# Optimization experiments

Measured on AMD Instinct MI355X. Metric: run time of the kernel, lower is better.

The kernel has to match this reference:

```python
import jax, jax.numpy as jnp
import numpy as np
import math

D_EMBED = 128   # per-head dim (config.d_embed)
N_HEADS = 12
ROPE_BASE = 10000.0


def rope(x):
    # x: [B, H, S, D]; interleaved-pair rotary embedding on last dim
    B, H, S, D = x.shape
    half = D // 2
    inv_freq = 1.0 / (ROPE_BASE ** (jnp.arange(0, half, dtype=jnp.float32) * 2.0 / D))
    ang = jnp.arange(S, dtype=jnp.float32)[:, None] * inv_freq[None, :]  # [S, D/2]
    cos, sin = jnp.cos(ang), jnp.sin(ang)
    xp = x.reshape(B, H, S, half, 2)
    x1, x2 = xp[..., 0], xp[..., 1]
    o1 = x1 * cos - x2 * sin
    o2 = x1 * sin + x2 * cos
    return jnp.stack([o1, o2], axis=-1).reshape(B, H, S, D)


def setup_inputs() -> dict:
    key = jax.random.key(0)
    ks = jax.random.split(key, 5)
    B, S, E = 2, 2048, D_EMBED // 2
    inner = N_HEADS * D_EMBED
    sc = 0.02
    return {
        "q": jax.random.normal(ks[0], (B, S, E), dtype=jnp.float32),
        "Wq": jax.random.normal(ks[1], (inner, E), dtype=jnp.float32) * sc,
        "Wk": jax.random.normal(ks[2], (inner, E), dtype=jnp.float32) * sc,
        "Wv": jax.random.normal(ks[3], (inner, E), dtype=jnp.float32) * sc,
        "Wo": jax.random.normal(ks[4], (E, inner), dtype=jnp.float32) * sc,
    }


def reference(q, Wq, Wk, Wv, Wo):
    B, S, E = q.shape
    H, D = N_HEADS, D_EMBED
    scale = 1.0 / math.sqrt(D)

    def proj(x, W):
        return (x @ W.T).reshape(B, S, H, D).transpose(0, 2, 1, 3)  # [B,H,S,D]

    qh = rope(proj(q, Wq))
    kh = rope(proj(q, Wk))
    vh = proj(q, Wv)

    scores = jnp.einsum("bhsd,bhtd->bhst", qh, kh) * scale  # [B,H,S,S]
    causal = jnp.tril(jnp.ones((S, S), dtype=bool))
    scores = jnp.where(causal, scores, -jnp.inf)
    probs = jax.nn.softmax(scores, axis=-1)  # dropout omitted (eval mode)
    out = jnp.einsum("bhst,bhtd->bhsd", probs, vh)
    out = out.transpose(0, 2, 1, 3).reshape(B, S, H * D)
    return out @ Wo.T  # [B,S,E]
```

## Files before the change

kernel.cpp:

```cpp
#include <hip/hip_runtime.h>
#include <stdint.h>


typedef short v8s __attribute__((ext_vector_type(8)));
typedef unsigned int v4u __attribute__((ext_vector_type(4)));
typedef float v4f __attribute__((ext_vector_type(4)));
typedef float v16f __attribute__((ext_vector_type(16)));

#define MFMA16(a, b, c) __builtin_amdgcn_mfma_f32_16x16x32_bf16(a, b, c, 0, 0, 0)
#define MFMA32(a, b, c) __builtin_amdgcn_mfma_f32_32x32x16_bf16(a, b, c, 0, 0, 0)

#if __has_builtin(__builtin_amdgcn_exp2f)
#define EXP2(x) __builtin_amdgcn_exp2f(x)
#else
#define EXP2(x) exp2f(x)
#endif

#define SCALE2 (0.08838834764831845f * 1.4426950408889634f)

__device__ __forceinline__ unsigned short f2bf(float f) {
  uint32_t u = __builtin_bit_cast(uint32_t, f);
  u += 0x7FFFu + ((u >> 16) & 1u);
  return (unsigned short)(u >> 16);
}

__device__ __forceinline__ uint32_t packbf(float lo, float hi) {
  return __builtin_amdgcn_perm(__builtin_bit_cast(uint32_t, hi) + 0x8000u,
                               __builtin_bit_cast(uint32_t, lo) + 0x8000u,
                               0x07060302u);
}

__device__ __forceinline__ v16f zero16() {
  v16f z;
#pragma unroll
  for (int i = 0; i < 16; ++i) z[i] = 0.f;
  return z;
}

__device__ __forceinline__ void gl_lds16(const unsigned short* g, unsigned short* l) {
  __builtin_amdgcn_global_load_lds(
      (const __attribute__((address_space(1))) uint32_t*)g,
      (__attribute__((address_space(3))) uint32_t*)l, 16, 0, 0);
}

__global__ __launch_bounds__(256) void rope_table(float* __restrict__ cos_t,
                                                  float* __restrict__ sin_t) {
  int idx = blockIdx.x * 256 + threadIdx.x;
  if (idx >= 2048 * 64) return;
  int s = idx >> 6, f = idx & 63;
  float inv = exp2f((float)f * -0.20762050593046014f);
  float ang = (float)s * inv;
  float si, co;
  sincosf(ang, &si, &co);
  cos_t[idx] = co;
  sin_t[idx] = si;
}

__global__ __launch_bounds__(256) void proj_rope(
    const float* __restrict__ x, const float* __restrict__ Wq,
    const float* __restrict__ Wk, const float* __restrict__ Wv,
    const float* __restrict__ cos_t, const float* __restrict__ sin_t,
    unsigned short* __restrict__ qh, unsigned short* __restrict__ kh,
    unsigned short* __restrict__ vt) {
  const int wave = threadIdx.x >> 6, lane = threadIdx.x & 63;
  const int l16 = lane & 15, quad = lane >> 4;
  const int by = blockIdx.y;
  const int o_base = by * 64 + wave * 16;
  const int mat = o_base / 1536;
  const int inner0 = o_base % 1536;
  const int d0w = inner0 & 127;
  const float* Wsrc = (mat == 0) ? Wq : ((mat == 1) ? Wk : Wv);
  const float qscale = (mat == 0) ? SCALE2 : 1.0f;

  __shared__ __align__(16) unsigned short Lt[64][72];

  v8s wb[2];
  {
    const float* wr = Wsrc + (size_t)(inner0 + l16) * 64 + quad * 8;
#pragma unroll
    for (int s = 0; s < 2; ++s) {
      float4 a = *(const float4*)(wr + s * 32);
      float4 b = *(const float4*)(wr + s * 32 + 4);
      v8s t;
      t[0] = (short)f2bf(a.x); t[1] = (short)f2bf(a.y);
      t[2] = (short)f2bf(a.z); t[3] = (short)f2bf(a.w);
      t[4] = (short)f2bf(b.x); t[5] = (short)f2bf(b.y);
      t[6] = (short)f2bf(b.z); t[7] = (short)f2bf(b.w);
      wb[s] = t;
    }
  }

  const int d = d0w + l16;
  const int half = d >> 1;

#pragma unroll
  for (int i = 0; i < 4; ++i) {
    const int tok0 = blockIdx.x * 64 + i * 16;
    const float* xr = x + (size_t)(tok0 + l16) * 64 + quad * 8;
    v8s xa[2];
#pragma unroll
    for (int s = 0; s < 2; ++s) {
      float4 a = *(const float4*)(xr + s * 32);
      float4 b = *(const float4*)(xr + s * 32 + 4);
      v8s t;
      t[0] = (short)f2bf(a.x); t[1] = (short)f2bf(a.y);
      t[2] = (short)f2bf(a.z); t[3] = (short)f2bf(a.w);
      t[4] = (short)f2bf(b.x); t[5] = (short)f2bf(b.y);
      t[6] = (short)f2bf(b.z); t[7] = (short)f2bf(b.w);
      xa[s] = t;
    }
    v4f acc = {0.f, 0.f, 0.f, 0.f};
    acc = MFMA16(xa[0], wb[0], acc);
    acc = MFMA16(xa[1], wb[1], acc);

    if (mat < 2) {
#pragma unroll
      for (int r = 0; r < 4; ++r) {
        int sidx = (tok0 + quad * 4 + r) & 2047;
        float val = acc[r];
        float prt = __shfl_xor(val, 1);
        float co = cos_t[sidx * 64 + half];
        float si = sin_t[sidx * 64 + half];
        float rot = ((d & 1) == 0) ? (val * co - prt * si)
                                   : (prt * si + val * co);
        Lt[i * 16 + quad * 4 + r][wave * 16 + l16] = f2bf(rot * qscale);
      }
    } else {
#pragma unroll
      for (int r = 0; r < 4; ++r)
        Lt[wave * 16 + l16][i * 16 + quad * 4 + r] = f2bf(acc[r]);
    }
  }
  __syncthreads();

  const int matb = (by * 64) / 1536;
  const int innerb = (by * 64) % 1536;
  const int hb = innerb >> 7;
  const int d0b = innerb & 127;
  const int b = (blockIdx.x * 64) >> 11;
  const int tokbase = (blockIdx.x * 64) & 2047;
#pragma unroll
  for (int jj = 0; jj < 2; ++jj) {
    int cid = jj * 256 + threadIdx.x;
    int outer = cid >> 3, ic = cid & 7;
    v8s val = *(const v8s*)&Lt[outer][ic * 8];
    if (matb < 2) {
      unsigned short* dst = (matb == 0 ? qh : kh) +
          (((size_t)(b * 12 + hb)) * 2048 + tokbase + outer) * 128 + d0b + ic * 8;
      *(v8s*)dst = val;
    } else {
      unsigned short* dst = vt +
          (((size_t)(b * 12 + hb)) * 128 + d0b + outer) * 2048 + tokbase + ic * 8;
      *(v8s*)dst = val;
    }
  }
}

__global__ __launch_bounds__(256, 2) void attn(
    const unsigned short* __restrict__ qh, const unsigned short* __restrict__ kh,
    const unsigned short* __restrict__ vt, unsigned short* __restrict__ att,
    const float* __restrict__ Wo, unsigned short* __restrict__ wob) {
  const int bh = blockIdx.x;
  const int qb = 15 - (int)blockIdx.y;
  const int t = threadIdx.x;
  const int lane = t & 63;
  const int l31 = lane & 31, hh = lane >> 5;
  const int w = t >> 6;
  const int r0w = qb * 128 + w * 32;
  const int qrow = r0w + l31;
  const int rowmax = r0w + 31;

  const unsigned short* Qb = qh + (size_t)bh * 2048 * 128;
  const unsigned short* Kb = kh + (size_t)bh * 2048 * 128;
  const unsigned short* Vb = vt + (size_t)bh * 128 * 2048;

  __shared__ __align__(16) unsigned short Ktile[2][64 * 128];
  __shared__ __align__(16) unsigned short Vtile[2][128 * 64];

  v8s qa[8];
  {
    const unsigned short* qr = Qb + (size_t)(r0w + l31) * 128 + hh * 8;
#pragma unroll
    for (int ks = 0; ks < 8; ++ks) qa[ks] = *(const v8s*)(qr + ks * 16);
  }

  int offK[4], offV[4], ldsO[4];
#pragma unroll
  for (int j = 0; j < 4; ++j) {
    int flat = j * 256 + t;
    int kr = flat >> 4, kc = flat & 15;
    offK[j] = kr * 128 + ((kc ^ (kr & 15)) << 3);
    int vd = flat >> 3, vc = flat & 7;
    offV[j] = vd * 2048 + ((vc ^ (vd & 7)) << 3);
    ldsO[j] = flat << 3;
  }
  auto stage = [&](int kt, int buf) {
    const int key0 = kt << 6;
    const unsigned short* kg = Kb + (size_t)key0 * 128;
    const unsigned short* vg = Vb + key0;
#pragma unroll
    for (int j = 0; j < 4; ++j) {
      gl_lds16(kg + offK[j], &Ktile[buf][ldsO[j]]);
      gl_lds16(vg + offV[j], &Vtile[buf][ldsO[j]]);
    }
  };

  v16f O[4];
#pragma unroll
  for (int i = 0; i < 4; ++i) O[i] = zero16();
  float lsum = 0.f;

  const int nkt = 2 * qb + 2;
  stage(0, 0);

  for (int kt = 0; kt < nkt; ++kt) {
    __syncthreads();
    if (kt + 1 < nkt) stage(kt + 1, (kt + 1) & 1);
    const int key0 = kt << 6;
    if (key0 > rowmax) continue;
    const unsigned short* Kl = Ktile[kt & 1];
    const unsigned short* Vl = Vtile[kt & 1];
    const bool hi = (key0 + 32) <= rowmax;
    const bool mask0 = (key0 + 31) > r0w;
    const bool mask1 = (key0 + 63) > r0w;

    auto softpack = [&](const v16f& S, int kh2, bool needmask, uint32_t* W) {
#pragma unroll
      for (int m = 0; m < 8; ++m) {
        float pa = EXP2(S[2 * m]);
        float pb = EXP2(S[2 * m + 1]);
        if (needmask) {
          int keyb = key0 + kh2 * 32 + 2 * (m & 1) + 8 * (m >> 1) + 4 * hh;
          pa = (keyb <= qrow) ? pa : 0.f;
          pb = (keyb + 1 <= qrow) ? pb : 0.f;
        }
        lsum += pa + pb;
        W[m] = packbf(pa, pb);
      }
    };
    auto pv = [&](const uint32_t* W, int kh2) {
      uint32_t r0 = __shfl_xor(hh ? W[0] : W[2], 32);
      uint32_t r1 = __shfl_xor(hh ? W[1] : W[3], 32);
      uint32_t r2 = __shfl_xor(hh ? W[4] : W[6], 32);
      uint32_t r3 = __shfl_xor(hh ? W[5] : W[7], 32);
#pragma unroll
      for (int gl = 0; gl < 2; ++gl) {
        const int g = kh2 * 2 + gl;
        if (key0 + g * 16 > rowmax) continue;
        uint32_t rA = gl ? r2 : r0, rB = gl ? r3 : r1;
        v4u fw;
        fw.x = hh ? rA : W[4 * gl];
        fw.y = hh ? rB : W[4 * gl + 1];
        fw.z = hh ? W[4 * gl + 2] : rA;
        fw.w = hh ? W[4 * gl + 3] : rB;
        v8s pb = __builtin_bit_cast(v8s, fw);
#pragma unroll
        for (int dt = 0; dt < 4; ++dt) {
          v8s va = *(const v8s*)(
              Vl + (((dt * 32 + l31) * 8 + ((2 * g + hh) ^ (l31 & 7))) << 3));
          O[dt] = MFMA32(va, pb, O[dt]);
        }
      }
    };

    v16f S0 = zero16();
#pragma unroll
    for (int ks = 0; ks < 8; ++ks) {
      v8s ka = *(const v8s*)(
          Kl + ((l31 * 16 + ((2 * ks + hh) ^ (l31 & 15))) << 3));
      S0 = MFMA32(ka, qa[ks], S0);
    }
    uint32_t W0[8];
    softpack(S0, 0, mask0, W0);
    pv(W0, 0);
    if (hi) {
      v16f S1 = zero16();
#pragma unroll
      for (int ks = 0; ks < 8; ++ks) {
        v8s ka = *(const v8s*)(
            Kl + (((32 + l31) * 16 + ((2 * ks + hh) ^ (l31 & 15))) << 3));
        S1 = MFMA32(ka, qa[ks], S1);
      }
      uint32_t W1[8];
      softpack(S1, 1, mask1, W1);
      pv(W1, 1);
    }
  }

  float tot = lsum + __shfl_xor(lsum, 32);
  float inv = 1.0f / tot;
  const int b = bh / 12, hq = bh % 12;
  unsigned short* arow = att + ((size_t)b * 2048 + qrow) * 1536 + hq * 128;
#pragma unroll
  for (int dt = 0; dt < 4; ++dt) {
#pragma unroll
    for (int pr = 0; pr < 4; ++pr) {
      float a0 = O[dt][4 * pr + 0] * inv, a1 = O[dt][4 * pr + 1] * inv;
      float a2 = O[dt][4 * pr + 2] * inv, a3 = O[dt][4 * pr + 3] * inv;
      uint2 uu;
      uu.x = packbf(a0, a1);
      uu.y = packbf(a2, a3);
      *(uint2*)(arow + dt * 32 + 8 * pr + 4 * hh) = uu;
    }
  }

  if (qb == 0) {
    const int base = bh * 4096;
#pragma unroll
    for (int i = 0; i < 16; ++i) wob[base + i * 256 + t] = f2bf(Wo[base + i * 256 + t]);
  }
}

__global__ __launch_bounds__(256) void outproj(
    const unsigned short* __restrict__ att, const unsigned short* __restrict__ wob,
    float* __restrict__ out) {
  const int wave = threadIdx.x >> 6, lane = threadIdx.x & 63;
  const int l16 = lane & 15, quad = lane >> 4;
  const int tok0 = blockIdx.x * 16;
  const int e0 = wave * 16;

  v4f acc0 = {0.f, 0.f, 0.f, 0.f}, acc1 = {0.f, 0.f, 0.f, 0.f};
  const unsigned short* ar = att + (size_t)(tok0 + l16) * 1536 + quad * 8;
  const unsigned short* wr = wob + (size_t)(e0 + l16) * 1536 + quad * 8;
#pragma unroll 4
  for (int s = 0; s < 24; ++s) {
    v8s a0 = *(const v8s*)(ar + (2 * s) * 32);
    v8s b0 = *(const v8s*)(wr + (2 * s) * 32);
    v8s a1 = *(const v8s*)(ar + (2 * s + 1) * 32);
    v8s b1 = *(const v8s*)(wr + (2 * s + 1) * 32);
    acc0 = MFMA16(a0, b0, acc0);
    acc1 = MFMA16(a1, b1, acc1);
  }
#pragma unroll
  for (int r = 0; r < 4; ++r)
    out[(size_t)(tok0 + quad * 4 + r) * 64 + e0 + l16] = acc0[r] + acc1[r];
}

extern "C" void kernel_launch(void* const* d_in, const int* in_sizes, int n_in,
                              void* d_out, int out_size, void* d_ws,
                              size_t ws_size, hipStream_t stream) {
  const float* q  = (const float*)d_in[0];
  const float* Wq = (const float*)d_in[1];
  const float* Wk = (const float*)d_in[2];
  const float* Wv = (const float*)d_in[3];
  const float* Wo = (const float*)d_in[4];
  float* out = (float*)d_out;

  unsigned short* ws = (unsigned short*)d_ws;
  unsigned short* qh  = ws;
  unsigned short* kh  = ws + 6291456;
  unsigned short* vt  = ws + 12582912;
  unsigned short* att = ws + 18874368;
  float* cos_t = (float*)((char*)d_ws + 50331648);
  float* sin_t = cos_t + 131072;
  unsigned short* wob = (unsigned short*)cos_t;

  rope_table<<<512, 256, 0, stream>>>(cos_t, sin_t);
  proj_rope<<<dim3(64, 72), 256, 0, stream>>>(q, Wq, Wk, Wv, cos_t, sin_t,
                                              qh, kh, vt);
  attn<<<dim3(24, 16), 256, 0, stream>>>(qh, kh, vt, att, Wo, wob);
  outproj<<<256, 256, 0, stream>>>(att, wob, out);
}
```

Before: 194.4 us.

## Split attention into 64-row query blocks with 32-key tiles and balanced scheduling

Shrinks attention work-groups from 4 to 2 waves covering 64 query rows, so the grid grows from 384 to 768 blocks. A remapped block index orders query blocks so heavy and light causal blocks are interleaved across the launch. Key/value tiles are halved to 32 keys with adjusted LDS swizzles. The QK^T accumulation is split into two independent MFMA chains to expose more ILP. This aims at better CU occupancy and load balance on the causal triangle, at the cost of more K/V reloads per query row and more barriers.

```diff
diff --git a/kernel.cpp b/kernel.cpp
--- a/kernel.cpp
+++ b/kernel.cpp
@@ -156,17 +156,19 @@
   }
 }
 
-__global__ __launch_bounds__(256, 2) void attn(
+__global__ __launch_bounds__(128, 2) void attn(
     const unsigned short* __restrict__ qh, const unsigned short* __restrict__ kh,
     const unsigned short* __restrict__ vt, unsigned short* __restrict__ att,
     const float* __restrict__ Wo, unsigned short* __restrict__ wob) {
-  const int bh = blockIdx.x;
-  const int qb = 15 - (int)blockIdx.y;
+  const int n = blockIdx.x;
+  const int bh = n % 24;
+  const int y = n / 24;
+  const int j = (y >= 11 && y < 22) ? (y - 1) : (31 - y);
   const int t = threadIdx.x;
   const int lane = t & 63;
   const int l31 = lane & 31, hh = lane >> 5;
   const int w = t >> 6;
-  const int r0w = qb * 128 + w * 32;
+  const int r0w = j * 64 + w * 32;
   const int qrow = r0w + l31;
   const int rowmax = r0w + 31;
 
@@ -174,8 +176,8 @@
   const unsigned short* Kb = kh + (size_t)bh * 2048 * 128;
   const unsigned short* Vb = vt + (size_t)bh * 128 * 2048;
 
-  __shared__ __align__(16) unsigned short Ktile[2][64 * 128];
-  __shared__ __align__(16) unsigned short Vtile[2][128 * 64];
+  __shared__ __align__(16) unsigned short Ktile[2][32 * 128];
+  __shared__ __align__(16) unsigned short Vtile[2][128 * 32];
 
   v8s qa[8];
   {
@@ -186,22 +188,22 @@
 
   int offK[4], offV[4], ldsO[4];
 #pragma unroll
-  for (int j = 0; j < 4; ++j) {
-    int flat = j * 256 + t;
+  for (int i = 0; i < 4; ++i) {
+    int flat = i * 128 + t;
     int kr = flat >> 4, kc = flat & 15;
-    offK[j] = kr * 128 + ((kc ^ (kr & 15)) << 3);
-    int vd = flat >> 3, vc = flat & 7;
-    offV[j] = vd * 2048 + ((vc ^ (vd & 7)) << 3);
-    ldsO[j] = flat << 3;
+    offK[i] = kr * 128 + ((kc ^ (kr & 15)) << 3);
+    int vd = flat >> 2, vc = flat & 3;
+    offV[i] = vd * 2048 + ((vc ^ ((vd >> 1) & 3)) << 3);
+    ldsO[i] = flat << 3;
   }
   auto stage = [&](int kt, int buf) {
-    const int key0 = kt << 6;
+    const int key0 = kt << 5;
     const unsigned short* kg = Kb + (size_t)key0 * 128;
     const unsigned short* vg = Vb + key0;
 #pragma unroll
-    for (int j = 0; j < 4; ++j) {
-      gl_lds16(kg + offK[j], &Ktile[buf][ldsO[j]]);
-      gl_lds16(vg + offV[j], &Vtile[buf][ldsO[j]]);
+    for (int i = 0; i < 4; ++i) {
+      gl_lds16(kg + offK[i], &Ktile[buf][ldsO[i]]);
+      gl_lds16(vg + offV[i], &Vtile[buf][ldsO[i]]);
     }
   };
 
@@ -210,80 +212,63 @@
   for (int i = 0; i < 4; ++i) O[i] = zero16();
   float lsum = 0.f;
 
-  const int nkt = 2 * qb + 2;
+  const int nkt = 2 * j + 2;
   stage(0, 0);
 
   for (int kt = 0; kt < nkt; ++kt) {
     __syncthreads();
     if (kt + 1 < nkt) stage(kt + 1, (kt + 1) & 1);
-    const int key0 = kt << 6;
+    const int key0 = kt << 5;
     if (key0 > rowmax) continue;
     const unsigned short* Kl = Ktile[kt & 1];
     const unsigned short* Vl = Vtile[kt & 1];
-    const bool hi = (key0 + 32) <= rowmax;
     const bool mask0 = (key0 + 31) > r0w;
-    const bool mask1 = (key0 + 63) > r0w;
-
-    auto softpack = [&](const v16f& S, int kh2, bool needmask, uint32_t* W) {
-#pragma unroll
-      for (int m = 0; m < 8; ++m) {
-        float pa = EXP2(S[2 * m]);
-        float pb = EXP2(S[2 * m + 1]);
-        if (needmask) {
-          int keyb = key0 + kh2 * 32 + 2 * (m & 1) + 8 * (m >> 1) + 4 * hh;
-          pa = (keyb <= qrow) ? pa : 0.f;
-          pb = (keyb + 1 <= qrow) ? pb : 0.f;
-        }
-        lsum += pa + pb;
-        W[m] = packbf(pa, pb);
+
+    v16f Sa = zero16(), Sb = zero16();
+#pragma unroll
+    for (int ks = 0; ks < 8; ks += 2) {
+      v8s ka0 = *(const v8s*)(
+          Kl + ((l31 * 16 + ((2 * ks + hh) ^ (l31 & 15))) << 3));
+      v8s ka1 = *(const v8s*)(
+          Kl + ((l31 * 16 + ((2 * ks + 2 + hh) ^ (l31 & 15))) << 3));
+      Sa = MFMA32(ka0, qa[ks], Sa);
+      Sb = MFMA32(ka1, qa[ks + 1], Sb);
+    }
+
+    uint32_t W[8];
+#pragma unroll
+    for (int m = 0; m < 8; ++m) {
+      float pa = EXP2(Sa[2 * m] + Sb[2 * m]);
+      float pb = EXP2(Sa[2 * m + 1] + Sb[2 * m + 1]);
+      if (mask0) {
+        int keyb = key0 + 2 * (m & 1) + 8 * (m >> 1) + 4 * hh;
+        pa = (keyb <= qrow) ? pa : 0.f;
+        pb = (keyb + 1 <= qrow) ? pb : 0.f;
       }
-    };
-    auto pv = [&](const uint32_t* W, int kh2) {
-      uint32_t r0 = __shfl_xor(hh ? W[0] : W[2], 32);
-      uint32_t r1 = __shfl_xor(hh ? W[1] : W[3], 32);
-      uint32_t r2 = __shfl_xor(hh ? W[4] : W[6], 32);
-      uint32_t r3 = __shfl_xor(hh ? W[5] : W[7], 32);
-#pragma unroll
-      for (int gl = 0; gl < 2; ++gl) {
-        const int g = kh2 * 2 + gl;
-        if (key0 + g * 16 > rowmax) continue;
-        uint32_t rA = gl ? r2 : r0, rB = gl ? r3 : r1;
-        v4u fw;
-        fw.x = hh ? rA : W[4 * gl];
-        fw.y = hh ? rB : W[4 * gl + 1];
-        fw.z = hh ? W[4 * gl + 2] : rA;
-        fw.w = hh ? W[4 * gl + 3] : rB;
-        v8s pb = __builtin_bit_cast(v8s, fw);
-#pragma unroll
-        for (int dt = 0; dt < 4; ++dt) {
-          v8s va = *(const v8s*)(
-              Vl + (((dt * 32 + l31) * 8 + ((2 * g + hh) ^ (l31 & 7))) << 3));
-          O[dt] = MFMA32(va, pb, O[dt]);
-        }
+      lsum += pa + pb;
+      W[m] = packbf(pa, pb);
+    }
+
+    uint32_t r0 = __shfl_xor(hh ? W[0] : W[2], 32);
+    uint32_t r1 = __shfl_xor(hh ? W[1] : W[3], 32);
+    uint32_t r2 = __shfl_xor(hh ? W[4] : W[6], 32);
+    uint32_t r3 = __shfl_xor(hh ? W[5] : W[7], 32);
+#pragma unroll
+    for (int g = 0; g < 2; ++g) {
+      if (key0 + g * 16 > rowmax) continue;
+      uint32_t rA = g ? r2 : r0, rB = g ? r3 : r1;
+      v4u fw;
+      fw.x = hh ? rA : W[4 * g];
+      fw.y = hh ? rB : W[4 * g + 1];
+      fw.z = hh ? W[4 * g + 2] : rA;
+      fw.w = hh ? W[4 * g + 3] : rB;
+      v8s pfrag = __builtin_bit_cast(v8s, fw);
+#pragma unroll
+      for (int dt = 0; dt < 4; ++dt) {
+        v8s va = *(const v8s*)(
+            Vl + (((dt * 32 + l31) * 4 + ((2 * g + hh) ^ ((l31 >> 1) & 3))) << 3));
+        O[dt] = MFMA32(va, pfrag, O[dt]);
       }
-    };
-
-    v16f S0 = zero16();
-#pragma unroll
-    for (int ks = 0; ks < 8; ++ks) {
-      v8s ka = *(const v8s*)(
-          Kl + ((l31 * 16 + ((2 * ks + hh) ^ (l31 & 15))) << 3));
-      S0 = MFMA32(ka, qa[ks], S0);
-    }
-    uint32_t W0[8];
-    softpack(S0, 0, mask0, W0);
-    pv(W0, 0);
-    if (hi) {
-      v16f S1 = zero16();
-#pragma unroll
-      for (int ks = 0; ks < 8; ++ks) {
-        v8s ka = *(const v8s*)(
-            Kl + (((32 + l31) * 16 + ((2 * ks + hh) ^ (l31 & 15))) << 3));
-        S1 = MFMA32(ka, qa[ks], S1);
-      }
-      uint32_t W1[8];
-      softpack(S1, 1, mask1, W1);
-      pv(W1, 1);
     }
   }
 
@@ -304,10 +289,10 @@
     }
   }
 
-  if (qb == 0) {
+  if (j == 0) {
     const int base = bh * 4096;
 #pragma unroll
-    for (int i = 0; i < 16; ++i) wob[base + i * 256 + t] = f2bf(Wo[base + i * 256 + t]);
+    for (int i = 0; i < 32; ++i) wob[base + i * 128 + t] = f2bf(Wo[base + i * 128 + t]);
   }
 }
 
@@ -358,6 +343,6 @@
   rope_table<<<512, 256, 0, stream>>>(cos_t, sin_t);
   proj_rope<<<dim3(64, 72), 256, 0, stream>>>(q, Wq, Wk, Wv, cos_t, sin_t,
                                               qh, kh, vt);
-  attn<<<dim3(24, 16), 256, 0, stream>>>(qh, kh, vt, att, Wo, wob);
+  attn<<<dim3(768), 128, 0, stream>>>(qh, kh, vt, att, Wo, wob);
   outproj<<<256, 256, 0, stream>>>(att, wob, out);
 }
```

Result: slower. 208.6 us (+7.3%).

## Prepack V into MFMA fragment layout and load directly to registers; triple-buffer K

Applied to the files above, without the earlier changes.

The projection kernel now writes V in a fragment-major layout so each attention wave can fetch its PV operands straight from global memory into registers, skipping the LDS V tile entirely. K staging becomes a three-deep ring with explicit vmcnt waits and a raw s_barrier instead of __syncthreads, which lets loads run two tiles ahead. The QK^T chain is split into two independent accumulators to shorten the MFMA dependency chain, and s_setprio is raised around the MFMA blocks. The risks are redundant global V reads across the four waves, more register pressure from the prefetched V fragments, and fragile hand-written wait counts.

```diff
diff --git a/kernel.cpp b/kernel.cpp
--- a/kernel.cpp
+++ b/kernel.cpp
@@ -149,8 +149,12 @@
           (((size_t)(b * 12 + hb)) * 2048 + tokbase + outer) * 128 + d0b + ic * 8;
       *(v8s*)dst = val;
     } else {
+      const int kt = tokbase >> 6;
+      const int G = ic >> 1, hhb = ic & 1;
+      const int dd = d0b + outer;
       unsigned short* dst = vt +
-          (((size_t)(b * 12 + hb)) * 128 + d0b + outer) * 2048 + tokbase + ic * 8;
+          ((((((size_t)(b * 12 + hb)) * 32 + kt) * 4 + G) * 4 + (dd >> 5)) * 64 +
+           hhb * 32 + (dd & 31)) * 8;
       *(v8s*)dst = val;
     }
   }
@@ -158,7 +162,7 @@
 
 __global__ __launch_bounds__(256, 2) void attn(
     const unsigned short* __restrict__ qh, const unsigned short* __restrict__ kh,
-    const unsigned short* __restrict__ vt, unsigned short* __restrict__ att,
+    const unsigned short* __restrict__ vtf, unsigned short* __restrict__ att,
     const float* __restrict__ Wo, unsigned short* __restrict__ wob) {
   const int bh = blockIdx.x;
   const int qb = 15 - (int)blockIdx.y;
@@ -172,10 +176,9 @@
 
   const unsigned short* Qb = qh + (size_t)bh * 2048 * 128;
   const unsigned short* Kb = kh + (size_t)bh * 2048 * 128;
-  const unsigned short* Vb = vt + (size_t)bh * 128 * 2048;
-
-  __shared__ __align__(16) unsigned short Ktile[2][64 * 128];
-  __shared__ __align__(16) unsigned short Vtile[2][128 * 64];
+  const unsigned short* Vb = vtf + (size_t)bh * 262144;
+
+  __shared__ __align__(16) unsigned short Ktile[3][64 * 128];
 
   v8s qa[8];
   {
@@ -184,25 +187,18 @@
     for (int ks = 0; ks < 8; ++ks) qa[ks] = *(const v8s*)(qr + ks * 16);
   }
 
-  int offK[4], offV[4], ldsO[4];
-#pragma unroll
-  for (int j = 0; j < 4; ++j) {
-    int flat = j * 256 + t;
+  int offK[4], ldsO[4];
+#pragma unroll
+  for (int i = 0; i < 4; ++i) {
+    int flat = i * 256 + t;
     int kr = flat >> 4, kc = flat & 15;
-    offK[j] = kr * 128 + ((kc ^ (kr & 15)) << 3);
-    int vd = flat >> 3, vc = flat & 7;
-    offV[j] = vd * 2048 + ((vc ^ (vd & 7)) << 3);
-    ldsO[j] = flat << 3;
-  }
-  auto stage = [&](int kt, int buf) {
-    const int key0 = kt << 6;
-    const unsigned short* kg = Kb + (size_t)key0 * 128;
-    const unsigned short* vg = Vb + key0;
-#pragma unroll
-    for (int j = 0; j < 4; ++j) {
-      gl_lds16(kg + offK[j], &Ktile[buf][ldsO[j]]);
-      gl_lds16(vg + offV[j], &Vtile[buf][ldsO[j]]);
-    }
+    offK[i] = kr * 128 + ((kc ^ (kr & 15)) << 3);
+    ldsO[i] = flat << 3;
+  }
+  auto stageK = [&](int kt, int buf) {
+    const unsigned short* kg = Kb + ((size_t)(kt << 6)) * 128;
+#pragma unroll
+    for (int i = 0; i < 4; ++i) gl_lds16(kg + offK[i], &Ktile[buf][ldsO[i]]);
   };
 
   v16f O[4];
@@ -211,24 +207,56 @@
   float lsum = 0.f;
 
   const int nkt = 2 * qb + 2;
-  stage(0, 0);
+  stageK(0, 0);
+  stageK(1, 1);
+  asm volatile("s_waitcnt vmcnt(4)" ::: "memory");
 
   for (int kt = 0; kt < nkt; ++kt) {
-    __syncthreads();
-    if (kt + 1 < nkt) stage(kt + 1, (kt + 1) & 1);
+    __builtin_amdgcn_s_barrier();
+    __builtin_amdgcn_sched_barrier(0);
     const int key0 = kt << 6;
-    if (key0 > rowmax) continue;
-    const unsigned short* Kl = Ktile[kt & 1];
-    const unsigned short* Vl = Vtile[kt & 1];
+    const bool active = key0 <= rowmax;
     const bool hi = (key0 + 32) <= rowmax;
+
+    v8s v0a[4], v0b[4], v1a[4], v1b[4];
+    if (active) {
+      const unsigned short* Vt = Vb + (size_t)kt * 8192;
+#pragma unroll
+      for (int dt = 0; dt < 4; ++dt)
+        v0a[dt] = *(const v8s*)(Vt + ((0 * 4 + dt) * 64 + lane) * 8);
+#pragma unroll
+      for (int dt = 0; dt < 4; ++dt)
+        v0b[dt] = *(const v8s*)(Vt + ((1 * 4 + dt) * 64 + lane) * 8);
+      if (hi) {
+#pragma unroll
+        for (int dt = 0; dt < 4; ++dt)
+          v1a[dt] = *(const v8s*)(Vt + ((2 * 4 + dt) * 64 + lane) * 8);
+#pragma unroll
+        for (int dt = 0; dt < 4; ++dt)
+          v1b[dt] = *(const v8s*)(Vt + ((3 * 4 + dt) * 64 + lane) * 8);
+      }
+    }
+    __builtin_amdgcn_sched_barrier(0);
+
+    if (kt + 2 < nkt) stageK(kt + 2, (kt + 2) % 3);
+    __builtin_amdgcn_sched_barrier(0);
+
+    if (!active) {
+      if (kt + 2 < nkt) asm volatile("s_waitcnt vmcnt(4)" ::: "memory");
+      else              asm volatile("s_waitcnt vmcnt(0)" ::: "memory");
+      continue;
+    }
+
+    const unsigned short* Kl = Ktile[kt % 3];
     const bool mask0 = (key0 + 31) > r0w;
     const bool mask1 = (key0 + 63) > r0w;
 
-    auto softpack = [&](const v16f& S, int kh2, bool needmask, uint32_t* W) {
+    auto softpack = [&](const v16f& SS, const v16f& ST, int kh2, bool needmask,
+                        uint32_t* W) {
 #pragma unroll
       for (int m = 0; m < 8; ++m) {
-        float pa = EXP2(S[2 * m]);
-        float pb = EXP2(S[2 * m + 1]);
+        float pa = EXP2(SS[2 * m] + ST[2 * m]);
+        float pb = EXP2(SS[2 * m + 1] + ST[2 * m + 1]);
         if (needmask) {
           int keyb = key0 + kh2 * 32 + 2 * (m & 1) + 8 * (m >> 1) + 4 * hh;
           pa = (keyb <= qrow) ? pa : 0.f;
@@ -238,7 +266,7 @@
         W[m] = packbf(pa, pb);
       }
     };
-    auto pv = [&](const uint32_t* W, int kh2) {
+    auto pvhalf = [&](const uint32_t* W, int kh2, const v8s* vA, const v8s* vB) {
       uint32_t r0 = __shfl_xor(hh ? W[0] : W[2], 32);
       uint32_t r1 = __shfl_xor(hh ? W[1] : W[3], 32);
       uint32_t r2 = __shfl_xor(hh ? W[4] : W[6], 32);
@@ -253,37 +281,47 @@
         fw.y = hh ? rB : W[4 * gl + 1];
         fw.z = hh ? W[4 * gl + 2] : rA;
         fw.w = hh ? W[4 * gl + 3] : rB;
-        v8s pb = __builtin_bit_cast(v8s, fw);
-#pragma unroll
-        for (int dt = 0; dt < 4; ++dt) {
-          v8s va = *(const v8s*)(
-              Vl + (((dt * 32 + l31) * 8 + ((2 * g + hh) ^ (l31 & 7))) << 3));
-          O[dt] = MFMA32(va, pb, O[dt]);
-        }
+        v8s pfrag = __builtin_bit_cast(v8s, fw);
+        const v8s* vv = gl ? vB : vA;
+        __builtin_amdgcn_s_setprio(1);
+#pragma unroll
+        for (int dt = 0; dt < 4; ++dt) O[dt] = MFMA32(vv[dt], pfrag, O[dt]);
+        __builtin_amdgcn_s_setprio(0);
       }
     };
 
-    v16f S0 = zero16();
-#pragma unroll
-    for (int ks = 0; ks < 8; ++ks) {
-      v8s ka = *(const v8s*)(
+    v16f Sa = zero16(), Sb = zero16();
+    __builtin_amdgcn_s_setprio(1);
+#pragma unroll
+    for (int ks = 0; ks < 8; ks += 2) {
+      v8s ka0 = *(const v8s*)(
           Kl + ((l31 * 16 + ((2 * ks + hh) ^ (l31 & 15))) << 3));
-      S0 = MFMA32(ka, qa[ks], S0);
-    }
+      v8s ka1 = *(const v8s*)(
+          Kl + ((l31 * 16 + ((2 * ks + 2 + hh) ^ (l31 & 15))) << 3));
+      Sa = MFMA32(ka0, qa[ks], Sa);
+      Sb = MFMA32(ka1, qa[ks + 1], Sb);
+    }
+    __builtin_amdgcn_s_setprio(0);
     uint32_t W0[8];
-    softpack(S0, 0, mask0, W0);
-    pv(W0, 0);
+    softpack(Sa, Sb, 0, mask0, W0);
+    pvhalf(W0, 0, v0a, v0b);
+
     if (hi) {
-      v16f S1 = zero16();
-#pragma unroll
-      for (int ks = 0; ks < 8; ++ks) {
-        v8s ka = *(const v8s*)(
+      v16f Sc = zero16(), Sd = zero16();
+      __builtin_amdgcn_s_setprio(1);
+#pragma unroll
+      for (int ks = 0; ks < 8; ks += 2) {
+        v8s ka0 = *(const v8s*)(
             Kl + (((32 + l31) * 16 + ((2 * ks + hh) ^ (l31 & 15))) << 3));
-        S1 = MFMA32(ka, qa[ks], S1);
+        v8s ka1 = *(const v8s*)(
+            Kl + (((32 + l31) * 16 + ((2 * ks + 2 + hh) ^ (l31 & 15))) << 3));
+        Sc = MFMA32(ka0, qa[ks], Sc);
+        Sd = MFMA32(ka1, qa[ks + 1], Sd);
       }
+      __builtin_amdgcn_s_setprio(0);
       uint32_t W1[8];
-      softpack(S1, 1, mask1, W1);
-      pv(W1, 1);
+      softpack(Sc, Sd, 1, mask1, W1);
+      pvhalf(W1, 1, v1a, v1b);
     }
   }
 
@@ -349,7 +387,7 @@
   unsigned short* ws = (unsigned short*)d_ws;
   unsigned short* qh  = ws;
   unsigned short* kh  = ws + 6291456;
-  unsigned short* vt  = ws + 12582912;
+  unsigned short* vtf = ws + 12582912;
   unsigned short* att = ws + 18874368;
   float* cos_t = (float*)((char*)d_ws + 50331648);
   float* sin_t = cos_t + 131072;
@@ -357,7 +395,7 @@
 
   rope_table<<<512, 256, 0, stream>>>(cos_t, sin_t);
   proj_rope<<<dim3(64, 72), 256, 0, stream>>>(q, Wq, Wk, Wv, cos_t, sin_t,
-                                              qh, kh, vt);
-  attn<<<dim3(24, 16), 256, 0, stream>>>(qh, kh, vt, att, Wo, wob);
+                                              qh, kh, vtf);
+  attn<<<dim3(24, 16), 256, 0, stream>>>(qh, kh, vtf, att, Wo, wob);
   outproj<<<256, 256, 0, stream>>>(att, wob, out);
 }
```

Result: slower. 200.9 us (+3.3%).
